# Kernel optimization log

Hardware: AMD Instinct MI355X
Metric: run time of the kernel (lower is better)

## Reference

```python
import jax, jax.numpy as jnp
import numpy as np

B, S, D, H = 4, 2048, 1024, 16
Dh = D // H


def _layernorm(x, a, b):
    # torch.var default is unbiased (ddof=1)
    mu = jnp.mean(x, axis=-1, keepdims=True)
    sg = jnp.var(x, axis=-1, keepdims=True, ddof=1)
    return (x - mu) / jnp.sqrt(sg + 1e-08) * a + b


def setup_inputs() -> dict:
    key = jax.random.key(0)
    ks = jax.random.split(key, 16)
    s = 1.0 / np.sqrt(D)
    inp = {
        'q': jax.random.normal(ks[0], (B, S, D), jnp.float32),
        'k': jax.random.normal(ks[1], (B, S, D), jnp.float32),
        'v': jax.random.normal(ks[2], (B, S, D), jnp.float32),
        'g': jax.random.normal(ks[3], (B, S, D), jnp.float32),
        # causal mask: True = masked
        'm': jnp.triu(jnp.ones((S, S), jnp.bool_), k=1)[None, None],
        'Wq': jax.random.uniform(ks[4], (D, D), jnp.float32, -s, s),
        'bq': jnp.zeros((D,), jnp.float32),
        'Wk': jax.random.uniform(ks[5], (D, D), jnp.float32, -s, s),
        'bk': jnp.zeros((D,), jnp.float32),
        'Wv': jax.random.uniform(ks[6], (D, D), jnp.float32, -s, s),
        'bv': jnp.zeros((D,), jnp.float32),
        'Wg': jax.random.uniform(ks[7], (D, D), jnp.float32, -s, s),
        'bg': jnp.zeros((D,), jnp.float32),
        'ln_a': jnp.ones((D,), jnp.float32),
        'ln_b': jnp.zeros((D,), jnp.float32),
        'Wo': jax.random.uniform(ks[8], (D, D), jnp.float32, -s, s),
        'bo': jnp.zeros((D,), jnp.float32),
    }
    return inp


def reference(q, k, v, g, m, Wq, bq, Wk, bk, Wv, bv, Wg, bg, ln_a, ln_b, Wo, bo):
    qp = q @ Wq.T + bq
    kp = k @ Wk.T + bk
    vp = v @ Wv.T + bv
    gp = g @ Wg.T + bg
    # gating path: exact GELU (torch default), then custom LayerNorm (unbiased var)
    vp = jax.nn.gelu(vp, approximate=False)
    gp = jax.nn.gelu(gp, approximate=False)
    vp = _layernorm(vp, ln_a, ln_b)
    # [B,S,D] -> [B,H,S,Dh]
    qh = qp.reshape(B, S, H, Dh).transpose(0, 2, 1, 3)
    kh = kp.reshape(B, S, H, Dh).transpose(0, 2, 1, 3)
    vh = vp.reshape(B, S, H, Dh).transpose(0, 2, 1, 3)
    gh = gp.reshape(B, S, H, Dh).transpose(0, 2, 1, 3)
    a = jnp.einsum('bhqd,bhkd->bhqk', qh, kh) / jnp.sqrt(jnp.float32(Dh))
    a = jnp.where(m, -jnp.inf, a)
    a = jax.nn.softmax(a, axis=-1)
    # dropout = 0.0 (inference): no-op
    o = jnp.einsum('bhqk,bhkd->bhqd', a, vh)
    o = o * gh
    o = o.transpose(0, 2, 1, 3).reshape(B, S, D)
    o = o @ Wo.T + bo
    return (o, a)
```

## Files before the change

### kernel.cpp

```cpp
#include <hip/hip_runtime.h>
#include <hip/hip_bf16.h>
#include <cstdint>
#include <cstddef>

#define DEVINL static __device__ __forceinline__

typedef short bf16x8 __attribute__((ext_vector_type(8)));
typedef short s16x4  __attribute__((ext_vector_type(4)));
typedef float f32x4  __attribute__((ext_vector_type(4)));
typedef unsigned short u16;

static constexpr int Bb = 4, Ss = 2048, Dd = 1024, Hh = 16;
static constexpr int Mrows = Bb * Ss;
static constexpr int BHc = Bb * Hh;

DEVINL u16 f2bf(float f) {
    union { float f; uint32_t u; } v; v.f = f;
    uint32_t r = v.u + 0x7fffu + ((v.u >> 16) & 1u);
    return (u16)(r >> 16);
}
DEVINL float bf2f(u16 h) {
    union { uint32_t u; float f; } v; v.u = ((uint32_t)h) << 16;
    return v.f;
}
DEVINL float gelu_exact(float x) {
    return 0.5f * x * (1.0f + erff(x * 0.70710678118654752f));
}
DEVINL void gload16(const u16* gsrc, u16* ldsdst) {
    auto* g = reinterpret_cast<const __attribute__((address_space(1))) uint32_t*>(
        reinterpret_cast<uintptr_t>(gsrc));
    auto* l = reinterpret_cast<__attribute__((address_space(3))) uint32_t*>(
        reinterpret_cast<uintptr_t>(ldsdst));
    __builtin_amdgcn_global_load_lds(g, l, 16, 0, 0);
}

__global__ __launch_bounds__(256) void k_cvt_in(
    const float* __restrict__ s0, const float* __restrict__ s1,
    const float* __restrict__ s2, const float* __restrict__ s3,
    u16* __restrict__ d0, u16* __restrict__ d1,
    u16* __restrict__ d2, u16* __restrict__ d3, int n4) {
    int t = blockIdx.x * 256 + threadIdx.x;
    if (t >= n4) return;
    const float* s; u16* d;
    switch (blockIdx.y) {
        case 0: s = s0; d = d0; break;
        case 1: s = s1; d = d1; break;
        case 2: s = s2; d = d2; break;
        default: s = s3; d = d3; break;
    }
    float4 v = ((const float4*)s)[t];
    ushort4 o;
    o.x = f2bf(v.x); o.y = f2bf(v.y); o.z = f2bf(v.z); o.w = f2bf(v.w);
    ((ushort4*)d)[t] = o;
}

__global__ __launch_bounds__(256) void k_cvt_w(
    const float* __restrict__ s0, const float* __restrict__ s1,
    const float* __restrict__ s2, const float* __restrict__ s3,
    const float* __restrict__ s4,
    u16* __restrict__ d0, u16* __restrict__ d1, u16* __restrict__ d2,
    u16* __restrict__ d3, u16* __restrict__ d4, int n4) {
    int t = blockIdx.x * 256 + threadIdx.x;
    if (t >= n4) return;
    const float* s; u16* d;
    switch (blockIdx.y) {
        case 0: s = s0; d = d0; break;
        case 1: s = s1; d = d1; break;
        case 2: s = s2; d = d2; break;
        case 3: s = s3; d = d3; break;
        default: s = s4; d = d4; break;
    }
    float4 v = ((const float4*)s)[t];
    ushort4 o;
    o.x = f2bf(v.x); o.y = f2bf(v.y); o.z = f2bf(v.z); o.w = f2bf(v.w);
    ((ushort4*)d)[t] = o;
}

template<int EPI>
__global__ __launch_bounds__(256) void k_gemm_bt(
    const u16* __restrict__ Ap, const u16* __restrict__ Wp,
    const float* __restrict__ bias, void* __restrict__ Cp,
    int Nsz, int Ksz)
{
    __shared__ u16 As[128 * 32];
    __shared__ u16 Bs[128 * 32];
    const int tid = threadIdx.x, lane = tid & 63, w = tid >> 6;
    const int wm = w >> 1, wn = w & 1;
    const int m0 = blockIdx.y * 128, n0 = blockIdx.x * 128;
    const int g = lane >> 4, li = lane & 15;

    const f32x4 zero4 = {0.f, 0.f, 0.f, 0.f};
    f32x4 acc[4][4];
#pragma unroll
    for (int m = 0; m < 4; m++)
#pragma unroll
        for (int n = 0; n < 4; n++) acc[m][n] = zero4;

    for (int k0 = 0; k0 < Ksz; k0 += 32) {
        __syncthreads();
#pragma unroll
        for (int i = 0; i < 2; i++) {
            int chunk = (w * 2 + i) * 64 + lane;
            int row = chunk >> 2, cp = chunk & 3;
            gload16(Ap + (size_t)(m0 + row) * Ksz + k0 + ((cp ^ ((row >> 1) & 3)) << 3),
                    &As[(w * 2 + i) * 512]);
        }
#pragma unroll
        for (int i = 0; i < 2; i++) {
            int chunk = (w * 2 + i) * 64 + lane;
            int row = chunk >> 2, cp = chunk & 3;
            gload16(Wp + (size_t)(n0 + row) * Ksz + k0 + ((cp ^ ((row >> 1) & 3)) << 3),
                    &Bs[(w * 2 + i) * 512]);
        }
        __syncthreads();

        bf16x8 af[4], bfr[4];
#pragma unroll
        for (int m = 0; m < 4; m++) {
            int row = wm * 64 + m * 16 + li;
            af[m] = *(const bf16x8*)&As[row * 32 + ((g ^ ((row >> 1) & 3)) << 3)];
        }
#pragma unroll
        for (int n = 0; n < 4; n++) {
            int row = wn * 64 + n * 16 + li;
            bfr[n] = *(const bf16x8*)&Bs[row * 32 + ((g ^ ((row >> 1) & 3)) << 3)];
        }
#pragma unroll
        for (int m = 0; m < 4; m++)
#pragma unroll
            for (int n = 0; n < 4; n++)
                acc[m][n] = __builtin_amdgcn_mfma_f32_16x16x32_bf16(af[m], bfr[n], acc[m][n], 0, 0, 0);
    }

#pragma unroll
    for (int m = 0; m < 4; m++) {
#pragma unroll
        for (int n = 0; n < 4; n++) {
            int col = n0 + wn * 64 + n * 16 + li;
            float bv = bias[col];
#pragma unroll
            for (int r = 0; r < 4; r++) {
                int row = m0 + wm * 64 + m * 16 + g * 4 + r;
                float v = acc[m][n][r] + bv;
                if (EPI == 1 || EPI == 2) v = gelu_exact(v);
                if (EPI == 0 || EPI == 1)
                    ((u16*)Cp)[(size_t)row * Nsz + col] = f2bf(v);
                else
                    ((float*)Cp)[(size_t)row * Nsz + col] = v;
            }
        }
    }
}

__global__ __launch_bounds__(256) void k_ln(const float* __restrict__ vp,
                                            const float* __restrict__ la,
                                            const float* __restrict__ lb,
                                            u16* __restrict__ vh) {
    int row = blockIdx.x;
    const float* x = vp + (size_t)row * 1024;
    int tid = threadIdx.x;
    float4 v = ((const float4*)x)[tid];
    float s = v.x + v.y + v.z + v.w;
    float s2 = v.x * v.x + v.y * v.y + v.z * v.z + v.w * v.w;
#pragma unroll
    for (int off = 1; off < 64; off <<= 1) {
        s  += __shfl_xor(s, off, 64);
        s2 += __shfl_xor(s2, off, 64);
    }
    __shared__ float red[8];
    int w = tid >> 6, lane = tid & 63;
    if (lane == 0) { red[w] = s; red[4 + w] = s2; }
    __syncthreads();
    s  = red[0] + red[1] + red[2] + red[3];
    s2 = red[4] + red[5] + red[6] + red[7];
    float mu = s * (1.0f / 1024.0f);
    float var = (s2 - 1024.0f * mu * mu) * (1.0f / 1023.0f);
    float rs = rsqrtf(var + 1e-8f);
    float4 a4 = ((const float4*)la)[tid];
    float4 b4 = ((const float4*)lb)[tid];
    ushort4 o;
    o.x = f2bf((v.x - mu) * rs * a4.x + b4.x);
    o.y = f2bf((v.y - mu) * rs * a4.y + b4.y);
    o.z = f2bf((v.z - mu) * rs * a4.z + b4.z);
    o.w = f2bf((v.w - mu) * rs * a4.w + b4.w);
    ((ushort4*)(vh + (size_t)row * 1024))[tid] = o;
}

__global__ __launch_bounds__(256) void k_transpose(const u16* __restrict__ vh,
                                                   u16* __restrict__ vhT) {
    int bh = blockIdx.y, b = bh >> 4, h = bh & 15, s0 = blockIdx.x * 64;
    __shared__ u16 t[64 * 96];
    int tid = threadIdx.x;
#pragma unroll
    for (int j = 0; j < 2; j++) {
        int u = j * 256 + tid;
        int r = u >> 3, c8 = u & 7;
        bf16x8 v = *(const bf16x8*)(vh + ((size_t)(b * 2048 + s0 + r) * 1024 + h * 64 + c8 * 8));
        *(bf16x8*)&t[r * 96 + c8 * 8] = v;
    }
    __syncthreads();
#pragma unroll
    for (int j = 0; j < 2; j++) {
        int u = j * 256 + tid;
        int d = u >> 3, s8 = u & 7;
        bf16x8 vv;
#pragma unroll
        for (int jj = 0; jj < 8; jj++) vv[jj] = (short)t[(s8 * 8 + jj) * 96 + d];
        *(bf16x8*)(vhT + ((size_t)(bh * 64 + d) * 2048 + s0 + s8 * 8)) = vv;
    }
}

__global__ __launch_bounds__(512) void k_attn_stats(const u16* __restrict__ qp,
                                                    const u16* __restrict__ kp,
                                                    float* __restrict__ lsum) {
    __shared__ u16 Ks[128 * 64];
    const int tid = threadIdx.x, lane = tid & 63, w = tid >> 6;
    const int g = lane >> 4, li = lane & 15;
    const int bh = blockIdx.y, b = bh >> 4, h = bh & 15;
    const int bx = blockIdx.x, q0 = bx * 128;
    const int qrow = q0 + w * 16 + li;
    const u16* qbase = qp + ((size_t)(b * 2048 + qrow) * 1024 + h * 64 + g * 8);
    bf16x8 qa0 = *(const bf16x8*)qbase;
    bf16x8 qa1 = *(const bf16x8*)(qbase + 32);
    float l_run = 0.f;
    const u16* kbh = kp + ((size_t)(b * 2048) * 1024 + h * 64);
    const f32x4 zero4 = {0.f, 0.f, 0.f, 0.f};

    for (int kt = 0; kt <= bx; ++kt) {
        const int k0 = kt * 128;
        __syncthreads();
#pragma unroll
        for (int i = 0; i < 2; i++) {
            int id = (w * 2 + i) * 64 + lane;
            int r = id >> 3, cp = id & 7;
            gload16(kbh + (size_t)(k0 + r) * 1024 + ((cp ^ (r & 7)) << 3), &Ks[(w * 2 + i) * 512]);
        }
        __syncthreads();
        f32x4 sc[8];
#pragma unroll
        for (int n = 0; n < 8; n++) {
            int rb = n * 16 + li;
            const u16* kr = &Ks[rb * 64];
            bf16x8 kb0 = *(const bf16x8*)&kr[(g ^ (rb & 7)) << 3];
            bf16x8 kb1 = *(const bf16x8*)&kr[((g + 4) ^ (rb & 7)) << 3];
            f32x4 c = zero4;
            c = __builtin_amdgcn_mfma_f32_16x16x32_bf16(kb0, qa0, c, 0, 0, 0);
            c = __builtin_amdgcn_mfma_f32_16x16x32_bf16(kb1, qa1, c, 0, 0, 0);
            sc[n] = c;
        }
#pragma unroll
        for (int n = 0; n < 8; n++)
#pragma unroll
            for (int r = 0; r < 4; r++) {
                int col = k0 + n * 16 + g * 4 + r;
                l_run += (col <= qrow) ? __expf(sc[n][r] * 0.125f) : 0.0f;
            }
    }
    l_run += __shfl_xor(l_run, 16, 64);
    l_run += __shfl_xor(l_run, 32, 64);
    if (g == 0) lsum[(size_t)bh * 2048 + qrow] = l_run;
}

__global__ __launch_bounds__(512) void k_attn_pv(const u16* __restrict__ qp,
                                                 const u16* __restrict__ kp,
                                                 const u16* __restrict__ vhT,
                                                 const u16* __restrict__ gh,
                                                 const float* __restrict__ lsum,
                                                 float* __restrict__ aout,
                                                 u16* __restrict__ gated) {
    __shared__ u16 Ks[128 * 64];
    __shared__ u16 Vs[64 * 128];
    __shared__ short Ps[8 * 16 * 128];
    const int tid = threadIdx.x, lane = tid & 63, w = tid >> 6;
    const int g = lane >> 4, li = lane & 15;
    const int bh = blockIdx.y, b = bh >> 4, h = bh & 15;
    const int bx = blockIdx.x, q0 = bx * 128;
    const int qrow0 = q0 + w * 16;
    const int qrow = qrow0 + li;
    const u16* qbase = qp + ((size_t)(b * 2048 + qrow) * 1024 + h * 64 + g * 8);
    bf16x8 qa0 = *(const bf16x8*)qbase;
    bf16x8 qa1 = *(const bf16x8*)(qbase + 32);
    const float linv = 1.0f / lsum[(size_t)bh * 2048 + qrow];
    const f32x4 zero4 = {0.f, 0.f, 0.f, 0.f};
    f32x4 oacc[4];
#pragma unroll
    for (int n = 0; n < 4; n++) oacc[n] = zero4;
    float* arow = aout + (size_t)bh * 2048 * 2048;
    const u16* kbh = kp + ((size_t)(b * 2048) * 1024 + h * 64);
    const u16* vbh = vhT + (size_t)bh * 64 * 2048;

    for (int kt = bx + 1; kt < 16; ++kt) {
        float* tbase = arow + (size_t)q0 * 2048 + kt * 128;
#pragma unroll
        for (int i = 0; i < 8; i++) {
            int u = i * 512 + tid;
            int row = u >> 5, cu = u & 31;
            __builtin_nontemporal_store(zero4, (f32x4*)(tbase + (size_t)row * 2048 + cu * 4));
        }
    }

    short* Pw = &Ps[w * 2048];
    for (int kt = 0; kt <= bx; ++kt) {
        const int k0 = kt * 128;
        __syncthreads();
#pragma unroll
        for (int i = 0; i < 2; i++) {
            int id = (w * 2 + i) * 64 + lane;
            int r = id >> 3, cp = id & 7;
            gload16(kbh + (size_t)(k0 + r) * 1024 + ((cp ^ (r & 7)) << 3), &Ks[(w * 2 + i) * 512]);
        }
#pragma unroll
        for (int i = 0; i < 2; i++) {
            int id = (w * 2 + i) * 64 + lane;
            int r = id >> 4, cp = id & 15;
            gload16(vbh + (size_t)r * 2048 + k0 + ((cp ^ (r & 7)) << 3), &Vs[(w * 2 + i) * 512]);
        }
        __syncthreads();
        f32x4 sc[8];
#pragma unroll
        for (int n = 0; n < 8; n++) {
            int rb = n * 16 + li;
            const u16* kr = &Ks[rb * 64];
            bf16x8 kb0 = *(const bf16x8*)&kr[(g ^ (rb & 7)) << 3];
            bf16x8 kb1 = *(const bf16x8*)&kr[((g + 4) ^ (rb & 7)) << 3];
            f32x4 c = zero4;
            c = __builtin_amdgcn_mfma_f32_16x16x32_bf16(kb0, qa0, c, 0, 0, 0);
            c = __builtin_amdgcn_mfma_f32_16x16x32_bf16(kb1, qa1, c, 0, 0, 0);
            sc[n] = c;
        }
#pragma unroll
        for (int n = 0; n < 8; n++) {
#pragma unroll
            for (int r = 0; r < 4; r++) {
                int col = k0 + n * 16 + g * 4 + r;
                float p = (col <= qrow) ? __expf(sc[n][r] * 0.125f) * linv : 0.0f;
                sc[n][r] = p;
            }
            __builtin_nontemporal_store(sc[n],
                (f32x4*)(arow + (size_t)qrow * 2048 + k0 + n * 16 + g * 4));
            s16x4 pk;
#pragma unroll
            for (int r = 0; r < 4; r++) pk[r] = (short)f2bf(sc[n][r]);
            int chunk = n * 2 + (g >> 1);
            *(s16x4*)&Pw[li * 128 + ((chunk ^ (li & 7)) << 3) + (g & 1) * 4] = pk;
        }
#pragma unroll
        for (int ks = 0; ks < 4; ++ks) {
            int cl = ks * 4 + g;
            bf16x8 pa = *(const bf16x8*)&Pw[li * 128 + ((cl ^ (li & 7)) << 3)];
#pragma unroll
            for (int n = 0; n < 4; n++) {
                int vr = n * 16 + li;
                bf16x8 vb = *(const bf16x8*)&Vs[vr * 128 + ((cl ^ (vr & 7)) << 3)];
                oacc[n] = __builtin_amdgcn_mfma_f32_16x16x32_bf16(pa, vb, oacc[n], 0, 0, 0);
            }
        }
    }

#pragma unroll
    for (int n = 0; n < 4; n++) {
        int d8 = n * 2 + (li >> 3), wi = li & 7;
#pragma unroll
        for (int r = 0; r < 4; r++) {
            int lr = g * 4 + r;
            Pw[lr * 64 + ((d8 ^ (lr & 7)) << 3) + wi] = (short)f2bf(oacc[n][r]);
        }
    }
    const u16* ghb_base = gh + (size_t)(b * 2048) * 1024 + h * 64;
#pragma unroll
    for (int it = 0; it < 2; ++it) {
        int lr = it * 8 + (lane >> 3);
        int c8 = lane & 7;
        int rowq = qrow0 + lr;
        bf16x8 ov = *(const bf16x8*)&Pw[lr * 64 + ((c8 ^ (lr & 7)) << 3)];
        bf16x8 gv = *(const bf16x8*)(ghb_base + (size_t)rowq * 1024 + c8 * 8);
        bf16x8 outv;
#pragma unroll
        for (int j = 0; j < 8; j++)
            outv[j] = (short)f2bf(bf2f((u16)ov[j]) * bf2f((u16)gv[j]));
        *(bf16x8*)(gated + ((size_t)(b * 2048 + rowq)) * 1024 + h * 64 + c8 * 8) = outv;
    }
}

extern "C" void kernel_launch(void* const* d_in, const int* in_sizes, int n_in,
                              void* d_out, int out_size, void* d_ws, size_t ws_size,
                              hipStream_t stream) {
    const float* q  = (const float*)d_in[0];
    const float* k  = (const float*)d_in[1];
    const float* v  = (const float*)d_in[2];
    const float* g  = (const float*)d_in[3];
    const float* Wq = (const float*)d_in[5];
    const float* bq = (const float*)d_in[6];
    const float* Wk = (const float*)d_in[7];
    const float* bk = (const float*)d_in[8];
    const float* Wv = (const float*)d_in[9];
    const float* bv = (const float*)d_in[10];
    const float* Wg = (const float*)d_in[11];
    const float* bg = (const float*)d_in[12];
    const float* ln_a = (const float*)d_in[13];
    const float* ln_b = (const float*)d_in[14];
    const float* Wo = (const float*)d_in[15];
    const float* bo = (const float*)d_in[16];

    float* o_out = (float*)d_out;
    float* a_out = o_out + (size_t)Mrows * Dd;

    u16* qp    = (u16*)d_ws;
    u16* kpb   = qp    + (size_t)Mrows * Dd;
    u16* vhT   = kpb   + (size_t)Mrows * Dd;
    u16* ghb   = vhT   + (size_t)Mrows * Dd;
    u16* gated = ghb   + (size_t)Mrows * Dd;
    u16* Wo_bf = gated + (size_t)Mrows * Dd;
    float* lsum = (float*)(Wo_bf + (size_t)Dd * Dd);

    u16* Wq_bf = (u16*)a_out;
    u16* Wk_bf = Wq_bf + (size_t)Dd * Dd;
    u16* Wv_bf = Wk_bf + (size_t)Dd * Dd;
    u16* Wg_bf = Wv_bf + (size_t)Dd * Dd;
    u16* qb    = Wg_bf + (size_t)Dd * Dd;
    u16* kb2   = qb    + (size_t)Mrows * Dd;
    u16* vb    = kb2   + (size_t)Mrows * Dd;
    u16* gb    = vb    + (size_t)Mrows * Dd;
    float* vp  = (float*)(gb + (size_t)Mrows * Dd);
    u16* vh    = (u16*)(vp + (size_t)Mrows * Dd);

    {
        int n4w = Dd * Dd / 4;
        dim3 gw((n4w + 255) / 256, 5);
        k_cvt_w<<<gw, 256, 0, stream>>>(Wq, Wk, Wv, Wg, Wo,
                                        Wq_bf, Wk_bf, Wv_bf, Wg_bf, Wo_bf, n4w);
        int n4i = Mrows * Dd / 4;
        dim3 gi((n4i + 255) / 256, 4);
        k_cvt_in<<<gi, 256, 0, stream>>>(q, k, v, g, qb, kb2, vb, gb, n4i);
    }

    dim3 gg(Dd / 128, Mrows / 128);
    k_gemm_bt<0><<<gg, 256, 0, stream>>>(qb,  Wq_bf, bq, qp,  Dd, Dd);
    k_gemm_bt<0><<<gg, 256, 0, stream>>>(kb2, Wk_bf, bk, kpb, Dd, Dd);
    k_gemm_bt<2><<<gg, 256, 0, stream>>>(vb,  Wv_bf, bv, vp,  Dd, Dd);
    k_gemm_bt<1><<<gg, 256, 0, stream>>>(gb,  Wg_bf, bg, ghb, Dd, Dd);

    k_ln<<<Mrows, 256, 0, stream>>>(vp, ln_a, ln_b, vh);

    dim3 gt(Ss / 64, BHc);
    k_transpose<<<gt, 256, 0, stream>>>(vh, vhT);

    dim3 ga(Ss / 128, BHc);
    k_attn_stats<<<ga, 512, 0, stream>>>(qp, kpb, lsum);
    k_attn_pv<<<ga, 512, 0, stream>>>(qp, kpb, vhT, ghb, lsum, a_out, gated);

    k_gemm_bt<3><<<gg, 256, 0, stream>>>(gated, Wo_bf, bo, o_out, Dd, Dd);
}
```

Before: 676.6 us.

## Batch QKVG projections, fuse attention stats and PV with causal load balancing

Merges the four projection GEMMs into one launch, with a block-index remap that spreads work across XCDs. The separate row-sum kernel is folded into the attention kernel, which now recomputes QK^T in two passes. Each block takes a pair of query tiles (i and 15-i) so causal work is balanced across blocks. The K and V tiles are read straight from global memory instead of being staged through LDS, which removes barriers but may cost more global or cache traffic. The output GEMM uses the same remapped grid.

```diff
diff --git a/kernel.cpp b/kernel.cpp
--- a/kernel.cpp
+++ b/kernel.cpp
@@ -76,18 +76,33 @@
     ((ushort4*)d)[t] = o;
 }
 
-template<int EPI>
-__global__ __launch_bounds__(256) void k_gemm_bt(
-    const u16* __restrict__ Ap, const u16* __restrict__ Wp,
-    const float* __restrict__ bias, void* __restrict__ Cp,
-    int Nsz, int Ksz)
+__global__ __launch_bounds__(256) void k_proj(
+    const u16* __restrict__ qb, const u16* __restrict__ kb,
+    const u16* __restrict__ vb, const u16* __restrict__ gb,
+    const u16* __restrict__ Wqb, const u16* __restrict__ Wkb,
+    const u16* __restrict__ Wvb, const u16* __restrict__ Wgb,
+    const float* __restrict__ bqp, const float* __restrict__ bkp,
+    const float* __restrict__ bvp, const float* __restrict__ bgp,
+    u16* __restrict__ qp, u16* __restrict__ kpo,
+    float* __restrict__ vp, u16* __restrict__ ghb)
 {
     __shared__ u16 As[128 * 32];
     __shared__ u16 Bs[128 * 32];
     const int tid = threadIdx.x, lane = tid & 63, w = tid >> 6;
     const int wm = w >> 1, wn = w & 1;
-    const int m0 = blockIdx.y * 128, n0 = blockIdx.x * 128;
     const int g = lane >> 4, li = lane & 15;
+    const int orig = blockIdx.x;
+    const int lid = (orig & 7) * 256 + (orig >> 3);
+    const int z = lid >> 9, rem = lid & 511;
+    const int m0 = (rem >> 3) * 128, n0 = (rem & 7) * 128;
+
+    const u16 *Ap, *Wp; const float* bias;
+    switch (z) {
+        case 0: Ap = qb; Wp = Wqb; bias = bqp; break;
+        case 1: Ap = kb; Wp = Wkb; bias = bkp; break;
+        case 2: Ap = vb; Wp = Wvb; bias = bvp; break;
+        default: Ap = gb; Wp = Wgb; bias = bgp; break;
+    }
 
     const f32x4 zero4 = {0.f, 0.f, 0.f, 0.f};
     f32x4 acc[4][4];
@@ -96,20 +111,20 @@
 #pragma unroll
         for (int n = 0; n < 4; n++) acc[m][n] = zero4;
 
-    for (int k0 = 0; k0 < Ksz; k0 += 32) {
+    for (int k0 = 0; k0 < 1024; k0 += 32) {
         __syncthreads();
 #pragma unroll
         for (int i = 0; i < 2; i++) {
             int chunk = (w * 2 + i) * 64 + lane;
             int row = chunk >> 2, cp = chunk & 3;
-            gload16(Ap + (size_t)(m0 + row) * Ksz + k0 + ((cp ^ ((row >> 1) & 3)) << 3),
+            gload16(Ap + (size_t)(m0 + row) * 1024 + k0 + ((cp ^ ((row >> 1) & 3)) << 3),
                     &As[(w * 2 + i) * 512]);
         }
 #pragma unroll
         for (int i = 0; i < 2; i++) {
             int chunk = (w * 2 + i) * 64 + lane;
             int row = chunk >> 2, cp = chunk & 3;
-            gload16(Wp + (size_t)(n0 + row) * Ksz + k0 + ((cp ^ ((row >> 1) & 3)) << 3),
+            gload16(Wp + (size_t)(n0 + row) * 1024 + k0 + ((cp ^ ((row >> 1) & 3)) << 3),
                     &Bs[(w * 2 + i) * 512]);
         }
         __syncthreads();
@@ -142,11 +157,82 @@
             for (int r = 0; r < 4; r++) {
                 int row = m0 + wm * 64 + m * 16 + g * 4 + r;
                 float v = acc[m][n][r] + bv;
-                if (EPI == 1 || EPI == 2) v = gelu_exact(v);
-                if (EPI == 0 || EPI == 1)
-                    ((u16*)Cp)[(size_t)row * Nsz + col] = f2bf(v);
-                else
-                    ((float*)Cp)[(size_t)row * Nsz + col] = v;
+                size_t idx = (size_t)row * 1024 + col;
+                if (z == 0)      qp[idx]  = f2bf(v);
+                else if (z == 1) kpo[idx] = f2bf(v);
+                else if (z == 2) vp[idx]  = gelu_exact(v);
+                else             ghb[idx] = f2bf(gelu_exact(v));
+            }
+        }
+    }
+}
+
+__global__ __launch_bounds__(256) void k_gemm_f(
+    const u16* __restrict__ Ap, const u16* __restrict__ Wp,
+    const float* __restrict__ bias, float* __restrict__ Cp)
+{
+    __shared__ u16 As[128 * 32];
+    __shared__ u16 Bs[128 * 32];
+    const int tid = threadIdx.x, lane = tid & 63, w = tid >> 6;
+    const int wm = w >> 1, wn = w & 1;
+    const int g = lane >> 4, li = lane & 15;
+    const int orig = blockIdx.x;
+    const int lid = (orig & 7) * 64 + (orig >> 3);
+    const int m0 = (lid >> 3) * 128, n0 = (lid & 7) * 128;
+
+    const f32x4 zero4 = {0.f, 0.f, 0.f, 0.f};
+    f32x4 acc[4][4];
+#pragma unroll
+    for (int m = 0; m < 4; m++)
+#pragma unroll
+        for (int n = 0; n < 4; n++) acc[m][n] = zero4;
+
+    for (int k0 = 0; k0 < 1024; k0 += 32) {
+        __syncthreads();
+#pragma unroll
+        for (int i = 0; i < 2; i++) {
+            int chunk = (w * 2 + i) * 64 + lane;
+            int row = chunk >> 2, cp = chunk & 3;
+            gload16(Ap + (size_t)(m0 + row) * 1024 + k0 + ((cp ^ ((row >> 1) & 3)) << 3),
+                    &As[(w * 2 + i) * 512]);
+        }
+#pragma unroll
+        for (int i = 0; i < 2; i++) {
+            int chunk = (w * 2 + i) * 64 + lane;
+            int row = chunk >> 2, cp = chunk & 3;
+            gload16(Wp + (size_t)(n0 + row) * 1024 + k0 + ((cp ^ ((row >> 1) & 3)) << 3),
+                    &Bs[(w * 2 + i) * 512]);
+        }
+        __syncthreads();
+
+        bf16x8 af[4], bfr[4];
+#pragma unroll
+        for (int m = 0; m < 4; m++) {
+            int row = wm * 64 + m * 16 + li;
+            af[m] = *(const bf16x8*)&As[row * 32 + ((g ^ ((row >> 1) & 3)) << 3)];
+        }
+#pragma unroll
+        for (int n = 0; n < 4; n++) {
+            int row = wn * 64 + n * 16 + li;
+            bfr[n] = *(const bf16x8*)&Bs[row * 32 + ((g ^ ((row >> 1) & 3)) << 3)];
+        }
+#pragma unroll
+        for (int m = 0; m < 4; m++)
+#pragma unroll
+            for (int n = 0; n < 4; n++)
+                acc[m][n] = __builtin_amdgcn_mfma_f32_16x16x32_bf16(af[m], bfr[n], acc[m][n], 0, 0, 0);
+    }
+
+#pragma unroll
+    for (int m = 0; m < 4; m++) {
+#pragma unroll
+        for (int n = 0; n < 4; n++) {
+            int col = n0 + wn * 64 + n * 16 + li;
+            float bv = bias[col];
+#pragma unroll
+            for (int r = 0; r < 4; r++) {
+                int row = m0 + wm * 64 + m * 16 + g * 4 + r;
+                Cp[(size_t)row * 1024 + col] = acc[m][n][r] + bv;
             }
         }
     }
@@ -210,175 +296,130 @@
     }
 }
 
-__global__ __launch_bounds__(512) void k_attn_stats(const u16* __restrict__ qp,
-                                                    const u16* __restrict__ kp,
-                                                    float* __restrict__ lsum) {
-    __shared__ u16 Ks[128 * 64];
-    const int tid = threadIdx.x, lane = tid & 63, w = tid >> 6;
-    const int g = lane >> 4, li = lane & 15;
-    const int bh = blockIdx.y, b = bh >> 4, h = bh & 15;
-    const int bx = blockIdx.x, q0 = bx * 128;
-    const int qrow = q0 + w * 16 + li;
-    const u16* qbase = qp + ((size_t)(b * 2048 + qrow) * 1024 + h * 64 + g * 8);
-    bf16x8 qa0 = *(const bf16x8*)qbase;
-    bf16x8 qa1 = *(const bf16x8*)(qbase + 32);
-    float l_run = 0.f;
-    const u16* kbh = kp + ((size_t)(b * 2048) * 1024 + h * 64);
-    const f32x4 zero4 = {0.f, 0.f, 0.f, 0.f};
-
-    for (int kt = 0; kt <= bx; ++kt) {
-        const int k0 = kt * 128;
-        __syncthreads();
-#pragma unroll
-        for (int i = 0; i < 2; i++) {
-            int id = (w * 2 + i) * 64 + lane;
-            int r = id >> 3, cp = id & 7;
-            gload16(kbh + (size_t)(k0 + r) * 1024 + ((cp ^ (r & 7)) << 3), &Ks[(w * 2 + i) * 512]);
-        }
-        __syncthreads();
-        f32x4 sc[8];
-#pragma unroll
-        for (int n = 0; n < 8; n++) {
-            int rb = n * 16 + li;
-            const u16* kr = &Ks[rb * 64];
-            bf16x8 kb0 = *(const bf16x8*)&kr[(g ^ (rb & 7)) << 3];
-            bf16x8 kb1 = *(const bf16x8*)&kr[((g + 4) ^ (rb & 7)) << 3];
-            f32x4 c = zero4;
-            c = __builtin_amdgcn_mfma_f32_16x16x32_bf16(kb0, qa0, c, 0, 0, 0);
-            c = __builtin_amdgcn_mfma_f32_16x16x32_bf16(kb1, qa1, c, 0, 0, 0);
-            sc[n] = c;
-        }
-#pragma unroll
-        for (int n = 0; n < 8; n++)
-#pragma unroll
-            for (int r = 0; r < 4; r++) {
-                int col = k0 + n * 16 + g * 4 + r;
-                l_run += (col <= qrow) ? __expf(sc[n][r] * 0.125f) : 0.0f;
-            }
-    }
-    l_run += __shfl_xor(l_run, 16, 64);
-    l_run += __shfl_xor(l_run, 32, 64);
-    if (g == 0) lsum[(size_t)bh * 2048 + qrow] = l_run;
-}
-
-__global__ __launch_bounds__(512) void k_attn_pv(const u16* __restrict__ qp,
-                                                 const u16* __restrict__ kp,
-                                                 const u16* __restrict__ vhT,
-                                                 const u16* __restrict__ gh,
-                                                 const float* __restrict__ lsum,
-                                                 float* __restrict__ aout,
-                                                 u16* __restrict__ gated) {
-    __shared__ u16 Ks[128 * 64];
-    __shared__ u16 Vs[64 * 128];
+__global__ __launch_bounds__(512) void k_attn(const u16* __restrict__ qp,
+                                              const u16* __restrict__ kp,
+                                              const u16* __restrict__ vhT,
+                                              const u16* __restrict__ gh,
+                                              float* __restrict__ aout,
+                                              u16* __restrict__ gated) {
     __shared__ short Ps[8 * 16 * 128];
     const int tid = threadIdx.x, lane = tid & 63, w = tid >> 6;
     const int g = lane >> 4, li = lane & 15;
-    const int bh = blockIdx.y, b = bh >> 4, h = bh & 15;
-    const int bx = blockIdx.x, q0 = bx * 128;
-    const int qrow0 = q0 + w * 16;
-    const int qrow = qrow0 + li;
-    const u16* qbase = qp + ((size_t)(b * 2048 + qrow) * 1024 + h * 64 + g * 8);
-    bf16x8 qa0 = *(const bf16x8*)qbase;
-    bf16x8 qa1 = *(const bf16x8*)(qbase + 32);
-    const float linv = 1.0f / lsum[(size_t)bh * 2048 + qrow];
-    const f32x4 zero4 = {0.f, 0.f, 0.f, 0.f};
-    f32x4 oacc[4];
-#pragma unroll
-    for (int n = 0; n < 4; n++) oacc[n] = zero4;
-    float* arow = aout + (size_t)bh * 2048 * 2048;
+    const int orig = blockIdx.x;
+    const int lid = (orig & 7) * 64 + (orig >> 3);
+    const int bh = lid >> 3, i0 = lid & 7;
+    const int b = bh >> 4, h = bh & 15;
     const u16* kbh = kp + ((size_t)(b * 2048) * 1024 + h * 64);
     const u16* vbh = vhT + (size_t)bh * 64 * 2048;
-
-    for (int kt = bx + 1; kt < 16; ++kt) {
-        float* tbase = arow + (size_t)q0 * 2048 + kt * 128;
-#pragma unroll
-        for (int i = 0; i < 8; i++) {
-            int u = i * 512 + tid;
-            int row = u >> 5, cu = u & 31;
-            __builtin_nontemporal_store(zero4, (f32x4*)(tbase + (size_t)row * 2048 + cu * 4));
-        }
-    }
-
+    const u16* ghb_base = gh + (size_t)(b * 2048) * 1024 + h * 64;
+    float* arow = aout + (size_t)bh * 2048 * 2048;
     short* Pw = &Ps[w * 2048];
-    for (int kt = 0; kt <= bx; ++kt) {
-        const int k0 = kt * 128;
-        __syncthreads();
-#pragma unroll
-        for (int i = 0; i < 2; i++) {
-            int id = (w * 2 + i) * 64 + lane;
-            int r = id >> 3, cp = id & 7;
-            gload16(kbh + (size_t)(k0 + r) * 1024 + ((cp ^ (r & 7)) << 3), &Ks[(w * 2 + i) * 512]);
-        }
-#pragma unroll
-        for (int i = 0; i < 2; i++) {
-            int id = (w * 2 + i) * 64 + lane;
-            int r = id >> 4, cp = id & 15;
-            gload16(vbh + (size_t)r * 2048 + k0 + ((cp ^ (r & 7)) << 3), &Vs[(w * 2 + i) * 512]);
-        }
-        __syncthreads();
-        f32x4 sc[8];
-#pragma unroll
-        for (int n = 0; n < 8; n++) {
-            int rb = n * 16 + li;
-            const u16* kr = &Ks[rb * 64];
-            bf16x8 kb0 = *(const bf16x8*)&kr[(g ^ (rb & 7)) << 3];
-            bf16x8 kb1 = *(const bf16x8*)&kr[((g + 4) ^ (rb & 7)) << 3];
-            f32x4 c = zero4;
-            c = __builtin_amdgcn_mfma_f32_16x16x32_bf16(kb0, qa0, c, 0, 0, 0);
-            c = __builtin_amdgcn_mfma_f32_16x16x32_bf16(kb1, qa1, c, 0, 0, 0);
-            sc[n] = c;
-        }
-#pragma unroll
-        for (int n = 0; n < 8; n++) {
+    const f32x4 zero4 = {0.f, 0.f, 0.f, 0.f};
+
+    for (int half = 0; half < 2; ++half) {
+        const int bx = half ? (15 - i0) : i0;
+        const int q0 = bx * 128;
+        const int qrow0 = q0 + w * 16;
+        const int qrow = qrow0 + li;
+        const u16* qbase = qp + ((size_t)(b * 2048 + qrow) * 1024 + h * 64 + g * 8);
+        bf16x8 qa0 = *(const bf16x8*)qbase;
+        bf16x8 qa1 = *(const bf16x8*)(qbase + 32);
+
+        for (int kt = bx + 1; kt < 16; ++kt) {
+            float* tbase = arow + (size_t)q0 * 2048 + kt * 128;
+#pragma unroll
+            for (int i = 0; i < 8; i++) {
+                int u = i * 512 + tid;
+                int row = u >> 5, cu = u & 31;
+                __builtin_nontemporal_store(zero4, (f32x4*)(tbase + (size_t)row * 2048 + cu * 4));
+            }
+        }
+
+        float l_run = 0.f;
+        for (int kt = 0; kt <= bx; ++kt) {
+            const int k0 = kt * 128;
+#pragma unroll
+            for (int n = 0; n < 8; n++) {
+                int rb = k0 + n * 16 + li;
+                const u16* krow = kbh + (size_t)rb * 1024 + g * 8;
+                bf16x8 kb0 = *(const bf16x8*)krow;
+                bf16x8 kb1 = *(const bf16x8*)(krow + 32);
+                f32x4 c = zero4;
+                c = __builtin_amdgcn_mfma_f32_16x16x32_bf16(kb0, qa0, c, 0, 0, 0);
+                c = __builtin_amdgcn_mfma_f32_16x16x32_bf16(kb1, qa1, c, 0, 0, 0);
+#pragma unroll
+                for (int r = 0; r < 4; r++) {
+                    int col = k0 + n * 16 + g * 4 + r;
+                    l_run += (col <= qrow) ? __expf(c[r] * 0.125f) : 0.0f;
+                }
+            }
+        }
+        l_run += __shfl_xor(l_run, 16, 64);
+        l_run += __shfl_xor(l_run, 32, 64);
+        const float linv = 1.0f / l_run;
+
+        f32x4 oacc[4];
+#pragma unroll
+        for (int n = 0; n < 4; n++) oacc[n] = zero4;
+        for (int kt = 0; kt <= bx; ++kt) {
+            const int k0 = kt * 128;
+#pragma unroll
+            for (int n = 0; n < 8; n++) {
+                int rb = k0 + n * 16 + li;
+                const u16* krow = kbh + (size_t)rb * 1024 + g * 8;
+                bf16x8 kb0 = *(const bf16x8*)krow;
+                bf16x8 kb1 = *(const bf16x8*)(krow + 32);
+                f32x4 c = zero4;
+                c = __builtin_amdgcn_mfma_f32_16x16x32_bf16(kb0, qa0, c, 0, 0, 0);
+                c = __builtin_amdgcn_mfma_f32_16x16x32_bf16(kb1, qa1, c, 0, 0, 0);
+#pragma unroll
+                for (int r = 0; r < 4; r++) {
+                    int col = k0 + n * 16 + g * 4 + r;
+                    c[r] = (col <= qrow) ? __expf(c[r] * 0.125f) * linv : 0.0f;
+                }
+                __builtin_nontemporal_store(c,
+                    (f32x4*)(arow + (size_t)qrow * 2048 + k0 + n * 16 + g * 4));
+                s16x4 pk;
+#pragma unroll
+                for (int r = 0; r < 4; r++) pk[r] = (short)f2bf(c[r]);
+                int chunk = n * 2 + (g >> 1);
+                *(s16x4*)&Pw[li * 128 + ((chunk ^ (li & 7)) << 3) + (g & 1) * 4] = pk;
+            }
+#pragma unroll
+            for (int ks = 0; ks < 4; ++ks) {
+                int cl = ks * 4 + g;
+                bf16x8 pa = *(const bf16x8*)&Pw[li * 128 + ((cl ^ (li & 7)) << 3)];
+#pragma unroll
+                for (int n = 0; n < 4; n++) {
+                    int vr = n * 16 + li;
+                    bf16x8 vb = *(const bf16x8*)(vbh + (size_t)vr * 2048 + k0 + cl * 8);
+                    oacc[n] = __builtin_amdgcn_mfma_f32_16x16x32_bf16(pa, vb, oacc[n], 0, 0, 0);
+                }
+            }
+        }
+
+#pragma unroll
+        for (int n = 0; n < 4; n++) {
+            int d8 = n * 2 + (li >> 3), wi = li & 7;
 #pragma unroll
             for (int r = 0; r < 4; r++) {
-                int col = k0 + n * 16 + g * 4 + r;
-                float p = (col <= qrow) ? __expf(sc[n][r] * 0.125f) * linv : 0.0f;
-                sc[n][r] = p;
-            }
-            __builtin_nontemporal_store(sc[n],
-                (f32x4*)(arow + (size_t)qrow * 2048 + k0 + n * 16 + g * 4));
-            s16x4 pk;
-#pragma unroll
-            for (int r = 0; r < 4; r++) pk[r] = (short)f2bf(sc[n][r]);
-            int chunk = n * 2 + (g >> 1);
-            *(s16x4*)&Pw[li * 128 + ((chunk ^ (li & 7)) << 3) + (g & 1) * 4] = pk;
-        }
-#pragma unroll
-        for (int ks = 0; ks < 4; ++ks) {
-            int cl = ks * 4 + g;
-            bf16x8 pa = *(const bf16x8*)&Pw[li * 128 + ((cl ^ (li & 7)) << 3)];
-#pragma unroll
-            for (int n = 0; n < 4; n++) {
-                int vr = n * 16 + li;
-                bf16x8 vb = *(const bf16x8*)&Vs[vr * 128 + ((cl ^ (vr & 7)) << 3)];
-                oacc[n] = __builtin_amdgcn_mfma_f32_16x16x32_bf16(pa, vb, oacc[n], 0, 0, 0);
-            }
-        }
-    }
-
-#pragma unroll
-    for (int n = 0; n < 4; n++) {
-        int d8 = n * 2 + (li >> 3), wi = li & 7;
-#pragma unroll
-        for (int r = 0; r < 4; r++) {
-            int lr = g * 4 + r;
-            Pw[lr * 64 + ((d8 ^ (lr & 7)) << 3) + wi] = (short)f2bf(oacc[n][r]);
-        }
-    }
-    const u16* ghb_base = gh + (size_t)(b * 2048) * 1024 + h * 64;
-#pragma unroll
-    for (int it = 0; it < 2; ++it) {
-        int lr = it * 8 + (lane >> 3);
-        int c8 = lane & 7;
-        int rowq = qrow0 + lr;
-        bf16x8 ov = *(const bf16x8*)&Pw[lr * 64 + ((c8 ^ (lr & 7)) << 3)];
-        bf16x8 gv = *(const bf16x8*)(ghb_base + (size_t)rowq * 1024 + c8 * 8);
-        bf16x8 outv;
-#pragma unroll
-        for (int j = 0; j < 8; j++)
-            outv[j] = (short)f2bf(bf2f((u16)ov[j]) * bf2f((u16)gv[j]));
-        *(bf16x8*)(gated + ((size_t)(b * 2048 + rowq)) * 1024 + h * 64 + c8 * 8) = outv;
+                int lr = g * 4 + r;
+                Pw[lr * 64 + ((d8 ^ (lr & 7)) << 3) + wi] = (short)f2bf(oacc[n][r]);
+            }
+        }
+#pragma unroll
+        for (int it = 0; it < 2; ++it) {
+            int lr = it * 8 + (lane >> 3);
+            int c8 = lane & 7;
+            int rowq = qrow0 + lr;
+            bf16x8 ov = *(const bf16x8*)&Pw[lr * 64 + ((c8 ^ (lr & 7)) << 3)];
+            bf16x8 gv = *(const bf16x8*)(ghb_base + (size_t)rowq * 1024 + c8 * 8);
+            bf16x8 outv;
+#pragma unroll
+            for (int j = 0; j < 8; j++)
+                outv[j] = (short)f2bf(bf2f((u16)ov[j]) * bf2f((u16)gv[j]));
+            *(bf16x8*)(gated + ((size_t)(b * 2048 + rowq)) * 1024 + h * 64 + c8 * 8) = outv;
+        }
     }
 }
 
@@ -411,7 +452,6 @@
     u16* ghb   = vhT   + (size_t)Mrows * Dd;
     u16* gated = ghb   + (size_t)Mrows * Dd;
     u16* Wo_bf = gated + (size_t)Mrows * Dd;
-    float* lsum = (float*)(Wo_bf + (size_t)Dd * Dd);
 
     u16* Wq_bf = (u16*)a_out;
     u16* Wk_bf = Wq_bf + (size_t)Dd * Dd;
@@ -434,20 +474,17 @@
         k_cvt_in<<<gi, 256, 0, stream>>>(q, k, v, g, qb, kb2, vb, gb, n4i);
     }
 
-    dim3 gg(Dd / 128, Mrows / 128);
-    k_gemm_bt<0><<<gg, 256, 0, stream>>>(qb,  Wq_bf, bq, qp,  Dd, Dd);
-    k_gemm_bt<0><<<gg, 256, 0, stream>>>(kb2, Wk_bf, bk, kpb, Dd, Dd);
-    k_gemm_bt<2><<<gg, 256, 0, stream>>>(vb,  Wv_bf, bv, vp,  Dd, Dd);
-    k_gemm_bt<1><<<gg, 256, 0, stream>>>(gb,  Wg_bf, bg, ghb, Dd, Dd);
+    k_proj<<<2048, 256, 0, stream>>>(qb, kb2, vb, gb,
+                                     Wq_bf, Wk_bf, Wv_bf, Wg_bf,
+                                     bq, bk, bv, bg,
+                                     qp, kpb, vp, ghb);
 
     k_ln<<<Mrows, 256, 0, stream>>>(vp, ln_a, ln_b, vh);
 
     dim3 gt(Ss / 64, BHc);
     k_transpose<<<gt, 256, 0, stream>>>(vh, vhT);
 
-    dim3 ga(Ss / 128, BHc);
-    k_attn_stats<<<ga, 512, 0, stream>>>(qp, kpb, lsum);
-    k_attn_pv<<<ga, 512, 0, stream>>>(qp, kpb, vhT, ghb, lsum, a_out, gated);
-
-    k_gemm_bt<3><<<gg, 256, 0, stream>>>(gated, Wo_bf, bo, o_out, Dd, Dd);
-}
+    k_attn<<<512, 512, 0, stream>>>(qp, kpb, vhT, ghb, a_out, gated);
+
+    k_gemm_f<<<512, 256, 0, stream>>>(gated, Wo_bf, bo, o_out);
+}
```

Result: no change. 672.6 us (-0.6%).
